# Optimization experiments

Measured on AMD Instinct MI355X. Metric: run time of the kernel, lower is better.

Reference implementation:

```python
import jax, jax.numpy as jnp
import numpy as np

B, S, D = 8, 4096, 1024
H, DH = 16, 64
DM = H * DH  # d_model = 1024


def setup_inputs() -> dict:
    key = jax.random.key(0)
    k0, k1, k2, k3 = jax.random.split(key, 4)
    x = jax.random.uniform(k0, (B, S, D), dtype=jnp.float32)
    # nn.Linear weights (stored here pre-transposed as [in, out]).
    Wq = jax.random.normal(k1, (D, DM), dtype=jnp.float32) * 0.02
    Wkv = jax.random.normal(k2, (D, 2 * DM), dtype=jnp.float32) * 0.02
    Wlin = jax.random.normal(k3, (DM, DM), dtype=jnp.float32) * 0.02
    blin = jnp.zeros((DM,), dtype=jnp.float32)
    return {"x": x, "Wq": Wq, "Wkv": Wkv, "Wlin": Wlin, "blin": blin}


def reference(x, Wq, Wkv, Wlin, blin):
    scale = DH ** (-0.5)
    # projections; cond_dim=None => cond = x (self attention), mask=None
    q = (x @ Wq).reshape(B, S, H, DH)          # [B,S,H,DH]
    kv = (x @ Wkv).reshape(B, S, H, 2 * DH)    # [B,S,H,2*DH]
    k, v = kv[..., :DH], kv[..., DH:]
    # dual softmax: q over feature dim (scaled), k over sequence dim
    q = jax.nn.softmax(q, axis=-1) * scale
    k = jax.nn.softmax(k, axis=1)              # seq axis in BSHD layout
    # context = k^T @ v per (batch, head): [B,H,DH,DH]
    context = jnp.einsum('bshd,bshe->bhde', k, v)
    # out = q @ context: [B,S,H,DH]
    out = jnp.einsum('bshd,bhde->bshe', q, context).reshape(B, S, DM)
    return out @ Wlin + blin
```

## Files before the change

kernel.cpp:

```cpp
#include <hip/hip_runtime.h>
#include <hip/hip_bf16.h>
#include <cstdint>

using bf16 = __hip_bfloat16;
typedef __attribute__((ext_vector_type(8))) short bf16x8;
typedef __attribute__((ext_vector_type(4))) float f32x4;

struct alignas(16) B8 { bf16 h[8]; };
struct alignas(8)  B4 { bf16 h[4]; };

__device__ __forceinline__ void gll16(const void* g, void* l) {
  __builtin_amdgcn_global_load_lds((__attribute__((address_space(1))) void*)g,
                                   (__attribute__((address_space(3))) void*)l,
                                   16, 0, 0);
}

__global__ void cast_f32_bf16(const float* __restrict__ in, bf16* __restrict__ out, long long n) {
  long long i = ((long long)blockIdx.x * blockDim.x + threadIdx.x) * 8;
  if (i >= n) return;
  float4 v0 = *(const float4*)(in + i);
  float4 v1 = *(const float4*)(in + i + 4);
  B8 o;
  o.h[0] = __float2bfloat16(v0.x); o.h[1] = __float2bfloat16(v0.y);
  o.h[2] = __float2bfloat16(v0.z); o.h[3] = __float2bfloat16(v0.w);
  o.h[4] = __float2bfloat16(v1.x); o.h[5] = __float2bfloat16(v1.y);
  o.h[6] = __float2bfloat16(v1.z); o.h[7] = __float2bfloat16(v1.w);
  *(B8*)(out + i) = o;
}

__global__ void tcast(const float* __restrict__ W, bf16* __restrict__ WT, int K, int N) {
  __shared__ float tile[32][33];
  int k0 = blockIdx.y * 32, n0 = blockIdx.x * 32;
  int tx = threadIdx.x, ty = threadIdx.y;
  for (int yy = ty; yy < 32; yy += 8)
    tile[yy][tx] = W[(size_t)(k0 + yy) * N + n0 + tx];
  __syncthreads();
  for (int yy = ty; yy < 32; yy += 8)
    WT[(size_t)(n0 + yy) * K + k0 + tx] = __float2bfloat16(tile[tx][yy]);
}

constexpr int QKV_NT = 12;

__global__ __launch_bounds__(512, 2)
void gemm_qkv(const bf16* __restrict__ A, const bf16* __restrict__ BT,
              bf16* __restrict__ Yq, float* __restrict__ ctxAcc)
{
  __shared__ __align__(16) union {
    struct { bf16 a[4 * 8192]; bf16 b[4 * 8192]; } g;
    struct { bf16 ekT[2][16384]; bf16 vT[2][16384]; } c;
  } sm;

  const int t = threadIdx.x;
  const int wave = t >> 6, lane = t & 63;
  const int lr = lane & 15, kq = lane >> 4;
  const int wm = wave >> 2, wn = wave & 3;
  const int bm = (int)blockIdx.x / QKV_NT, bn = (int)blockIdx.x % QKV_NT;
  const int m0 = bm * 256, n0 = bn * 256;

  const int srow = t >> 2;
  const int cl = (t & 3) ^ ((srow ^ (srow >> 2)) & 3);
  const bf16* aop0 = A + (size_t)(m0 + srow) * 1024 + cl * 8;
  const bf16* aop1 = A + (size_t)(m0 + 128 + srow) * 1024 + cl * 8;
  const bf16* bop0 = BT + (size_t)(n0 + srow) * 1024 + cl * 8;
  const bf16* bop1 = BT + (size_t)(n0 + 128 + srow) * 1024 + cl * 8;
  bf16* const ldsA = sm.g.a;
  bf16* const ldsB = sm.g.b;
  const int wd0 = wave * 512;
  const int wd1 = 4096 + wave * 512;

  const int fc = (kq ^ ((lr ^ (lr >> 2)) & 3)) * 8;
  const int arow = wm * 128 + lr;
  const int brow = wn * 64 + lr;

#define STAGE_A(slot, ko) do { gll16(aop0 + (ko), ldsA + (slot) * 8192 + wd0); \
                               gll16(aop1 + (ko), ldsA + (slot) * 8192 + wd1); } while (0)
#define STAGE_B(slot, ko) do { gll16(bop0 + (ko), ldsB + (slot) * 8192 + wd0); \
                               gll16(bop1 + (ko), ldsB + (slot) * 8192 + wd1); } while (0)
#define AFRAG(slot, i) (*(const bf16x8*)(ldsA + (slot) * 8192 + (arow + (i) * 16) * 32 + fc))
#define BFRAG(slot, j) (*(const bf16x8*)(ldsB + (slot) * 8192 + (brow + (j) * 16) * 32 + fc))

  const f32x4 zero = {0.f, 0.f, 0.f, 0.f};
  f32x4 acc[8][4];
  #pragma unroll
  for (int i = 0; i < 8; i++)
    #pragma unroll
    for (int j = 0; j < 4; j++) acc[i][j] = zero;

  STAGE_A(0, 0); STAGE_B(0, 0);
  STAGE_A(1, 32); STAGE_B(1, 32);
  asm volatile("s_waitcnt vmcnt(4)" ::: "memory");
  __builtin_amdgcn_s_barrier();
  __builtin_amdgcn_sched_barrier(0);

  #pragma unroll 2
  for (int kt = 0; kt < 16; ++kt) {
    const int s0 = (2 * kt) & 3, s1 = (2 * kt + 1) & 3;
    const int p0 = (2 * kt + 2) & 3, p1 = (2 * kt + 3) & 3;
    const int ko = (kt + 1) * 64;
    const bool more = kt < 15;
    bf16x8 a[4], b[4];

    #pragma unroll
    for (int j = 0; j < 4; j++) b[j] = BFRAG(s0, j);
    #pragma unroll
    for (int i = 0; i < 4; i++) a[i] = AFRAG(s0, i);
    if (more) STAGE_A(p0, ko);
    __builtin_amdgcn_s_barrier();
    asm volatile("s_waitcnt lgkmcnt(0)" ::: "memory");
    __builtin_amdgcn_sched_barrier(0);
    __builtin_amdgcn_s_setprio(1);
    #pragma unroll
    for (int i = 0; i < 4; i++)
      #pragma unroll
      for (int j = 0; j < 4; j++)
        acc[i][j] = __builtin_amdgcn_mfma_f32_16x16x32_bf16(a[i], b[j], acc[i][j], 0, 0, 0);
    __builtin_amdgcn_s_setprio(0);
    __builtin_amdgcn_s_barrier();

    #pragma unroll
    for (int i = 0; i < 4; i++) a[i] = AFRAG(s0, i + 4);
    if (more) STAGE_B(p0, ko);
    __builtin_amdgcn_s_barrier();
    asm volatile("s_waitcnt lgkmcnt(0)" ::: "memory");
    __builtin_amdgcn_sched_barrier(0);
    __builtin_amdgcn_s_setprio(1);
    #pragma unroll
    for (int i = 0; i < 4; i++)
      #pragma unroll
      for (int j = 0; j < 4; j++)
        acc[i + 4][j] = __builtin_amdgcn_mfma_f32_16x16x32_bf16(a[i], b[j], acc[i + 4][j], 0, 0, 0);
    __builtin_amdgcn_s_setprio(0);
    if (more) { asm volatile("s_waitcnt vmcnt(4)" ::: "memory"); }
    else      { asm volatile("s_waitcnt vmcnt(0)" ::: "memory"); }
    __builtin_amdgcn_s_barrier();
    __builtin_amdgcn_sched_barrier(0);

    #pragma unroll
    for (int j = 0; j < 4; j++) b[j] = BFRAG(s1, j);
    #pragma unroll
    for (int i = 0; i < 4; i++) a[i] = AFRAG(s1, i);
    if (more) STAGE_A(p1, ko + 32);
    __builtin_amdgcn_s_barrier();
    asm volatile("s_waitcnt lgkmcnt(0)" ::: "memory");
    __builtin_amdgcn_sched_barrier(0);
    __builtin_amdgcn_s_setprio(1);
    #pragma unroll
    for (int i = 0; i < 4; i++)
      #pragma unroll
      for (int j = 0; j < 4; j++)
        acc[i][j] = __builtin_amdgcn_mfma_f32_16x16x32_bf16(a[i], b[j], acc[i][j], 0, 0, 0);
    __builtin_amdgcn_s_setprio(0);
    __builtin_amdgcn_s_barrier();

    #pragma unroll
    for (int i = 0; i < 4; i++) a[i] = AFRAG(s1, i + 4);
    if (more) STAGE_B(p1, ko + 32);
    __builtin_amdgcn_s_barrier();
    asm volatile("s_waitcnt lgkmcnt(0)" ::: "memory");
    __builtin_amdgcn_sched_barrier(0);
    __builtin_amdgcn_s_setprio(1);
    #pragma unroll
    for (int i = 0; i < 4; i++)
      #pragma unroll
      for (int j = 0; j < 4; j++)
        acc[i + 4][j] = __builtin_amdgcn_mfma_f32_16x16x32_bf16(a[i], b[j], acc[i + 4][j], 0, 0, 0);
    __builtin_amdgcn_s_setprio(0);
    if (more) { asm volatile("s_waitcnt vmcnt(4)" ::: "memory"); }
    else      { asm volatile("s_waitcnt vmcnt(0)" ::: "memory"); }
    __builtin_amdgcn_s_barrier();
    __builtin_amdgcn_sched_barrier(0);
  }

  if (bn < 4) {
    #pragma unroll
    for (int i = 0; i < 8; i++) {
      #pragma unroll
      for (int r = 0; r < 4; r++) {
        float m = fmaxf(fmaxf(acc[i][0][r], acc[i][1][r]),
                        fmaxf(acc[i][2][r], acc[i][3][r]));
        m = fmaxf(m, __shfl_xor(m, 1));
        m = fmaxf(m, __shfl_xor(m, 2));
        m = fmaxf(m, __shfl_xor(m, 4));
        m = fmaxf(m, __shfl_xor(m, 8));
        float ex[4]; float s = 0.f;
        #pragma unroll
        for (int j = 0; j < 4; j++) { ex[j] = __expf(acc[i][j][r] - m); s += ex[j]; }
        s += __shfl_xor(s, 1);
        s += __shfl_xor(s, 2);
        s += __shfl_xor(s, 4);
        s += __shfl_xor(s, 8);
        const float inv = 0.125f / s;
        const int row = m0 + wm * 128 + i * 16 + kq * 4 + r;
        bf16* yrow = Yq + (size_t)row * 1024 + n0 + wn * 64;
        #pragma unroll
        for (int j = 0; j < 4; j++)
          yrow[j * 16 + lr] = __float2bfloat16(ex[j] * inv);
      }
    }
  } else {
    const int bb = m0 >> 12;
    const int h0 = (n0 - 1024) >> 7;
    const int hloc = wn >> 1, isV = wn & 1;
    bf16* const dstT = (isV ? sm.c.vT[hloc] : sm.c.ekT[hloc]);

    float zp[4] = {0.f, 0.f, 0.f, 0.f};
    #pragma unroll
    for (int i = 0; i < 8; i++) {
      const int sbase = wm * 128 + i * 16 + kq * 4;
      const int sxo = sbase >> 3;
      const int sby = (sbase & 7) * 2;
      #pragma unroll
      for (int j = 0; j < 4; j++) {
        const int d = j * 16 + lr;
        B4 pk;
        if (!isV) {
          #pragma unroll
          for (int r = 0; r < 4; r++) {
            float e = __expf(acc[i][j][r]);
            zp[j] += e;
            pk.h[r] = __float2bfloat16(e);
          }
        } else {
          #pragma unroll
          for (int r = 0; r < 4; r++) pk.h[r] = __float2bfloat16(acc[i][j][r]);
        }
        *(B4*)((char*)dstT + d * 512 + ((sxo ^ (d & 7)) << 4) + sby) = pk;
      }
    }

    if (!isV) {
      #pragma unroll
      for (int j = 0; j < 4; j++) {
        zp[j] += __shfl_xor(zp[j], 16);
        zp[j] += __shfl_xor(zp[j], 32);
      }
      if (kq == 0) {
        float* zb = ctxAcc + (size_t)(bb * 16 + h0 + hloc) * 4160 + 4096;
        #pragma unroll
        for (int j = 0; j < 4; j++) atomicAdd(zb + j * 16 + lr, zp[j]);
      }
    }
    __syncthreads();

    const int hh = wave >> 2, dq = wave & 3;
    const bf16* const ek = sm.c.ekT[hh];
    const bf16* const vv = sm.c.vT[hh];
    f32x4 racc[4] = {zero, zero, zero, zero};
    #pragma unroll
    for (int ks = 0; ks < 8; ks++) {
      const int ch = ks * 4 + kq;
      bf16x8 af = *(const bf16x8*)((const char*)ek + (dq * 16 + lr) * 512 + ((ch ^ (lr & 7)) << 4));
      #pragma unroll
      for (int j = 0; j < 4; j++) {
        bf16x8 bfr = *(const bf16x8*)((const char*)vv + (j * 16 + lr) * 512 + ((ch ^ (lr & 7)) << 4));
        racc[j] = __builtin_amdgcn_mfma_f32_16x16x32_bf16(af, bfr, racc[j], 0, 0, 0);
      }
    }
    float* cb = ctxAcc + (size_t)(bb * 16 + h0 + hh) * 4160;
    #pragma unroll
    for (int j = 0; j < 4; j++) {
      #pragma unroll
      for (int r = 0; r < 4; r++)
        atomicAdd(cb + (dq * 16 + kq * 4 + r) * 64 + j * 16 + lr, racc[j][r]);
    }
  }
#undef STAGE_A
#undef STAGE_B
#undef AFRAG
#undef BFRAG
}

__global__ __launch_bounds__(256) void ctx_finish(const float* __restrict__ ctxAcc,
                                                  bf16* __restrict__ ctxN) {
  const int bh = blockIdx.x;
  const int t = threadIdx.x;
  __shared__ float zs[64];
  const float* src = ctxAcc + (size_t)bh * 4160;
  if (t < 64) zs[t] = src[4096 + t];
  __syncthreads();
  for (int idx = t; idx < 4096; idx += 256)
    ctxN[(size_t)bh * 4096 + idx] = __float2bfloat16(src[idx] / zs[idx >> 6]);
}

__global__ __launch_bounds__(256) void make_w2t(const bf16* __restrict__ ctxN,
                                                const bf16* __restrict__ WlinT,
                                                bf16* __restrict__ W2T) {
  const int nc = blockIdx.x;
  const int bh = blockIdx.y;
  const int b = bh >> 4, h = bh & 15;
  const int t = threadIdx.x, lane = t & 63, w = t >> 6;
  float creg[64];
  const bf16* crow = ctxN + (size_t)bh * 4096 + lane * 64;
  #pragma unroll
  for (int e8 = 0; e8 < 8; e8++) {
    B8 v = *(const B8*)(crow + e8 * 8);
    #pragma unroll
    for (int j = 0; j < 8; j++) creg[e8 * 8 + j] = __bfloat162float(v.h[j]);
  }
  for (int i = 0; i < 16; i++) {
    const int n = nc * 64 + w * 16 + i;
    const bf16* wrow = WlinT + (size_t)n * 1024 + h * 64;
    float acc = 0.f;
    #pragma unroll
    for (int e8 = 0; e8 < 8; e8++) {
      B8 v = *(const B8*)(wrow + e8 * 8);
      #pragma unroll
      for (int j = 0; j < 8; j++) acc += creg[e8 * 8 + j] * __bfloat162float(v.h[j]);
    }
    W2T[((size_t)b * 1024 + n) * 1024 + h * 64 + lane] = __float2bfloat16(acc);
  }
}

__global__ __launch_bounds__(256)
void gemm_out(const bf16* __restrict__ Aall, const bf16* __restrict__ BTall,
              float* __restrict__ Call, const float* __restrict__ bias)
{
  __shared__ __align__(16) bf16 As[128 * 32];
  __shared__ __align__(16) bf16 Bs[128 * 32];
  const int bz = blockIdx.y;
  const bf16* A  = Aall  + (size_t)bz * 4096 * 1024;
  const bf16* BT = BTall + (size_t)bz * 1024 * 1024;
  float* C       = Call  + (size_t)bz * 4096 * 1024;
  const int nt = 8;
  const int bm = (int)blockIdx.x / nt, bn = (int)blockIdx.x % nt;
  const int m0 = bm * 128, n0 = bn * 128;
  const int t = threadIdx.x;
  const int wave = t >> 6, lane = t & 63;
  const int lr = lane & 15, kq = lane >> 4, kb = kq * 8;
  const int wm = (wave >> 1) * 64, wn = (wave & 1) * 64;

  const int srow = t >> 2;
  const int scol = (t & 3) * 8;
  const bf16* a_src0 = A + (size_t)(m0 + srow) * 1024 + scol;
  const bf16* a_src1 = A + (size_t)(m0 + 64 + srow) * 1024 + scol;
  const bf16* b_src0 = BT + (size_t)(n0 + srow) * 1024 + scol;
  const bf16* b_src1 = BT + (size_t)(n0 + 64 + srow) * 1024 + scol;
  bf16* a_dst0 = As + wave * 512;
  bf16* a_dst1 = As + 2048 + wave * 512;
  bf16* b_dst0 = Bs + wave * 512;
  bf16* b_dst1 = Bs + 2048 + wave * 512;

  f32x4 zero = {0.f, 0.f, 0.f, 0.f};
  f32x4 acc[4][4];
  #pragma unroll
  for (int i = 0; i < 4; i++)
    #pragma unroll
    for (int j = 0; j < 4; j++) acc[i][j] = zero;

  for (int kt = 0; kt < 32; ++kt) {
    __syncthreads();
    gll16(a_src0, a_dst0); gll16(a_src1, a_dst1);
    gll16(b_src0, b_dst0); gll16(b_src1, b_dst1);
    a_src0 += 32; a_src1 += 32; b_src0 += 32; b_src1 += 32;
    __syncthreads();
    bf16x8 a[4], b[4];
    #pragma unroll
    for (int i = 0; i < 4; i++) a[i] = *(const bf16x8*)(As + (wm + i * 16 + lr) * 32 + kb);
    #pragma unroll
    for (int j = 0; j < 4; j++) b[j] = *(const bf16x8*)(Bs + (wn + j * 16 + lr) * 32 + kb);
    #pragma unroll
    for (int i = 0; i < 4; i++)
      #pragma unroll
      for (int j = 0; j < 4; j++)
        acc[i][j] = __builtin_amdgcn_mfma_f32_16x16x32_bf16(a[i], b[j], acc[i][j], 0, 0, 0);
  }

  #pragma unroll
  for (int i = 0; i < 4; i++) {
    const int row0 = m0 + wm + i * 16 + kq * 4;
    #pragma unroll
    for (int j = 0; j < 4; j++) {
      const int col = n0 + wn + j * 16 + lr;
      const float bv = bias[col];
      #pragma unroll
      for (int r = 0; r < 4; r++)
        C[(size_t)(row0 + r) * 1024 + col] = acc[i][j][r] + bv;
    }
  }
}

extern "C" void kernel_launch(void* const* d_in, const int* in_sizes, int n_in,
                              void* d_out, int out_size, void* d_ws, size_t ws_size,
                              hipStream_t stream) {
  (void)in_sizes; (void)n_in; (void)out_size; (void)ws_size;
  const float* x    = (const float*)d_in[0];
  const float* Wq   = (const float*)d_in[1];
  const float* Wkv  = (const float*)d_in[2];
  const float* Wlin = (const float*)d_in[3];
  const float* blin = (const float*)d_in[4];
  float* out = (float*)d_out;

  bf16* x_bf  = (bf16*)d_ws;
  bf16* WTc   = x_bf + 33554432;
  bf16* WlinT = WTc + 3145728;
  bf16* Yq    = WlinT + 1048576;
  bf16* ctxN  = Yq + 33554432;
  bf16* W2T   = ctxN + 524288;
  float* ctxAcc = (float*)(W2T + 8388608);

  cast_f32_bf16<<<16384, 256, 0, stream>>>(x, x_bf, 33554432LL);
  tcast<<<dim3(32, 32), dim3(32, 8), 0, stream>>>(Wq, WTc, 1024, 1024);
  tcast<<<dim3(64, 32), dim3(32, 8), 0, stream>>>(Wkv, WTc + 1048576, 1024, 2048);
  tcast<<<dim3(32, 32), dim3(32, 8), 0, stream>>>(Wlin, WlinT, 1024, 1024);

  hipMemsetAsync(ctxAcc, 0, (size_t)128 * 4160 * sizeof(float), stream);

  gemm_qkv<<<dim3(128 * QKV_NT), 512, 0, stream>>>(x_bf, WTc, Yq, ctxAcc);
  ctx_finish<<<128, 256, 0, stream>>>(ctxAcc, ctxN);
  make_w2t<<<dim3(16, 128), 256, 0, stream>>>(ctxN, WlinT, W2T);
  gemm_out<<<dim3(256, 8), 256, 0, stream>>>(Yq, W2T, out, blin);
}
```

Measured before the change: 439.4 us.

## Reuse pipelined 256x256 GEMM mainloop for output GEMM and fuse ctx normalization

Moves the four-slot, LDS-swizzled 256x256 MFMA mainloop of the QKV GEMM into a shared device function. The output GEMM now uses it with 512 threads, replacing the simple 128x128 tile that synchronised on every k-step. It also drops the ctx_finish kernel: make_w2t reads the fp32 context accumulators and divides by the normaliser inline, which saves a launch and an intermediate buffer. The larger tile launches fewer blocks (512) and uses more LDS and registers per block, so occupancy and wave balance change.

```diff
diff --git a/kernel.cpp b/kernel.cpp
--- a/kernel.cpp
+++ b/kernel.cpp
@@ -39,6 +39,109 @@
     WT[(size_t)(n0 + yy) * K + k0 + tx] = __float2bfloat16(tile[tx][yy]);
 }
 
+__device__ __forceinline__ void gemm_mainloop_256(
+    const bf16* __restrict__ aop0, const bf16* __restrict__ aop1,
+    const bf16* __restrict__ bop0, const bf16* __restrict__ bop1,
+    bf16* ldsA, bf16* ldsB, int wd0, int wd1,
+    int arow, int brow, int fc, f32x4 (&acc)[8][4])
+{
+#define STAGE_A(slot, ko) do { gll16(aop0 + (ko), ldsA + (slot) * 8192 + wd0); \
+                               gll16(aop1 + (ko), ldsA + (slot) * 8192 + wd1); } while (0)
+#define STAGE_B(slot, ko) do { gll16(bop0 + (ko), ldsB + (slot) * 8192 + wd0); \
+                               gll16(bop1 + (ko), ldsB + (slot) * 8192 + wd1); } while (0)
+#define AFRAG(slot, i) (*(const bf16x8*)(ldsA + (slot) * 8192 + (arow + (i) * 16) * 32 + fc))
+#define BFRAG(slot, j) (*(const bf16x8*)(ldsB + (slot) * 8192 + (brow + (j) * 16) * 32 + fc))
+
+  STAGE_A(0, 0); STAGE_B(0, 0);
+  STAGE_A(1, 32); STAGE_B(1, 32);
+  asm volatile("s_waitcnt vmcnt(4)" ::: "memory");
+  __builtin_amdgcn_s_barrier();
+  __builtin_amdgcn_sched_barrier(0);
+
+  #pragma unroll 2
+  for (int kt = 0; kt < 16; ++kt) {
+    const int s0 = (2 * kt) & 3, s1 = (2 * kt + 1) & 3;
+    const int p0 = (2 * kt + 2) & 3, p1 = (2 * kt + 3) & 3;
+    const int ko = (kt + 1) * 64;
+    const bool more = kt < 15;
+    bf16x8 a[4], b[4];
+
+    #pragma unroll
+    for (int j = 0; j < 4; j++) b[j] = BFRAG(s0, j);
+    #pragma unroll
+    for (int i = 0; i < 4; i++) a[i] = AFRAG(s0, i);
+    if (more) STAGE_A(p0, ko);
+    __builtin_amdgcn_s_barrier();
+    asm volatile("s_waitcnt lgkmcnt(0)" ::: "memory");
+    __builtin_amdgcn_sched_barrier(0);
+    __builtin_amdgcn_s_setprio(1);
+    #pragma unroll
+    for (int i = 0; i < 4; i++)
+      #pragma unroll
+      for (int j = 0; j < 4; j++)
+        acc[i][j] = __builtin_amdgcn_mfma_f32_16x16x32_bf16(a[i], b[j], acc[i][j], 0, 0, 0);
+    __builtin_amdgcn_s_setprio(0);
+    __builtin_amdgcn_s_barrier();
+
+    #pragma unroll
+    for (int i = 0; i < 4; i++) a[i] = AFRAG(s0, i + 4);
+    if (more) STAGE_B(p0, ko);
+    __builtin_amdgcn_s_barrier();
+    asm volatile("s_waitcnt lgkmcnt(0)" ::: "memory");
+    __builtin_amdgcn_sched_barrier(0);
+    __builtin_amdgcn_s_setprio(1);
+    #pragma unroll
+    for (int i = 0; i < 4; i++)
+      #pragma unroll
+      for (int j = 0; j < 4; j++)
+        acc[i + 4][j] = __builtin_amdgcn_mfma_f32_16x16x32_bf16(a[i], b[j], acc[i + 4][j], 0, 0, 0);
+    __builtin_amdgcn_s_setprio(0);
+    if (more) { asm volatile("s_waitcnt vmcnt(4)" ::: "memory"); }
+    else      { asm volatile("s_waitcnt vmcnt(0)" ::: "memory"); }
+    __builtin_amdgcn_s_barrier();
+    __builtin_amdgcn_sched_barrier(0);
+
+    #pragma unroll
+    for (int j = 0; j < 4; j++) b[j] = BFRAG(s1, j);
+    #pragma unroll
+    for (int i = 0; i < 4; i++) a[i] = AFRAG(s1, i);
+    if (more) STAGE_A(p1, ko + 32);
+    __builtin_amdgcn_s_barrier();
+    asm volatile("s_waitcnt lgkmcnt(0)" ::: "memory");
+    __builtin_amdgcn_sched_barrier(0);
+    __builtin_amdgcn_s_setprio(1);
+    #pragma unroll
+    for (int i = 0; i < 4; i++)
+      #pragma unroll
+      for (int j = 0; j < 4; j++)
+        acc[i][j] = __builtin_amdgcn_mfma_f32_16x16x32_bf16(a[i], b[j], acc[i][j], 0, 0, 0);
+    __builtin_amdgcn_s_setprio(0);
+    __builtin_amdgcn_s_barrier();
+
+    #pragma unroll
+    for (int i = 0; i < 4; i++) a[i] = AFRAG(s1, i + 4);
+    if (more) STAGE_B(p1, ko + 32);
+    __builtin_amdgcn_s_barrier();
+    asm volatile("s_waitcnt lgkmcnt(0)" ::: "memory");
+    __builtin_amdgcn_sched_barrier(0);
+    __builtin_amdgcn_s_setprio(1);
+    #pragma unroll
+    for (int i = 0; i < 4; i++)
+      #pragma unroll
+      for (int j = 0; j < 4; j++)
+        acc[i + 4][j] = __builtin_amdgcn_mfma_f32_16x16x32_bf16(a[i], b[j], acc[i + 4][j], 0, 0, 0);
+    __builtin_amdgcn_s_setprio(0);
+    if (more) { asm volatile("s_waitcnt vmcnt(4)" ::: "memory"); }
+    else      { asm volatile("s_waitcnt vmcnt(0)" ::: "memory"); }
+    __builtin_amdgcn_s_barrier();
+    __builtin_amdgcn_sched_barrier(0);
+  }
+#undef STAGE_A
+#undef STAGE_B
+#undef AFRAG
+#undef BFRAG
+}
+
 constexpr int QKV_NT = 12;
 
 __global__ __launch_bounds__(512, 2)
@@ -63,8 +166,6 @@
   const bf16* aop1 = A + (size_t)(m0 + 128 + srow) * 1024 + cl * 8;
   const bf16* bop0 = BT + (size_t)(n0 + srow) * 1024 + cl * 8;
   const bf16* bop1 = BT + (size_t)(n0 + 128 + srow) * 1024 + cl * 8;
-  bf16* const ldsA = sm.g.a;
-  bf16* const ldsB = sm.g.b;
   const int wd0 = wave * 512;
   const int wd1 = 4096 + wave * 512;
 
@@ -72,13 +173,6 @@
   const int arow = wm * 128 + lr;
   const int brow = wn * 64 + lr;
 
-#define STAGE_A(slot, ko) do { gll16(aop0 + (ko), ldsA + (slot) * 8192 + wd0); \
-                               gll16(aop1 + (ko), ldsA + (slot) * 8192 + wd1); } while (0)
-#define STAGE_B(slot, ko) do { gll16(bop0 + (ko), ldsB + (slot) * 8192 + wd0); \
-                               gll16(bop1 + (ko), ldsB + (slot) * 8192 + wd1); } while (0)
-#define AFRAG(slot, i) (*(const bf16x8*)(ldsA + (slot) * 8192 + (arow + (i) * 16) * 32 + fc))
-#define BFRAG(slot, j) (*(const bf16x8*)(ldsB + (slot) * 8192 + (brow + (j) * 16) * 32 + fc))
-
   const f32x4 zero = {0.f, 0.f, 0.f, 0.f};
   f32x4 acc[8][4];
   #pragma unroll
@@ -86,90 +180,8 @@
     #pragma unroll
     for (int j = 0; j < 4; j++) acc[i][j] = zero;
 
-  STAGE_A(0, 0); STAGE_B(0, 0);
-  STAGE_A(1, 32); STAGE_B(1, 32);
-  asm volatile("s_waitcnt vmcnt(4)" ::: "memory");
-  __builtin_amdgcn_s_barrier();
-  __builtin_amdgcn_sched_barrier(0);
-
-  #pragma unroll 2
-  for (int kt = 0; kt < 16; ++kt) {
-    const int s0 = (2 * kt) & 3, s1 = (2 * kt + 1) & 3;
-    const int p0 = (2 * kt + 2) & 3, p1 = (2 * kt + 3) & 3;
-    const int ko = (kt + 1) * 64;
-    const bool more = kt < 15;
-    bf16x8 a[4], b[4];
-
-    #pragma unroll
-    for (int j = 0; j < 4; j++) b[j] = BFRAG(s0, j);
-    #pragma unroll
-    for (int i = 0; i < 4; i++) a[i] = AFRAG(s0, i);
-    if (more) STAGE_A(p0, ko);
-    __builtin_amdgcn_s_barrier();
-    asm volatile("s_waitcnt lgkmcnt(0)" ::: "memory");
-    __builtin_amdgcn_sched_barrier(0);
-    __builtin_amdgcn_s_setprio(1);
-    #pragma unroll
-    for (int i = 0; i < 4; i++)
-      #pragma unroll
-      for (int j = 0; j < 4; j++)
-        acc[i][j] = __builtin_amdgcn_mfma_f32_16x16x32_bf16(a[i], b[j], acc[i][j], 0, 0, 0);
-    __builtin_amdgcn_s_setprio(0);
-    __builtin_amdgcn_s_barrier();
-
-    #pragma unroll
-    for (int i = 0; i < 4; i++) a[i] = AFRAG(s0, i + 4);
-    if (more) STAGE_B(p0, ko);
-    __builtin_amdgcn_s_barrier();
-    asm volatile("s_waitcnt lgkmcnt(0)" ::: "memory");
-    __builtin_amdgcn_sched_barrier(0);
-    __builtin_amdgcn_s_setprio(1);
-    #pragma unroll
-    for (int i = 0; i < 4; i++)
-      #pragma unroll
-      for (int j = 0; j < 4; j++)
-        acc[i + 4][j] = __builtin_amdgcn_mfma_f32_16x16x32_bf16(a[i], b[j], acc[i + 4][j], 0, 0, 0);
-    __builtin_amdgcn_s_setprio(0);
-    if (more) { asm volatile("s_waitcnt vmcnt(4)" ::: "memory"); }
-    else      { asm volatile("s_waitcnt vmcnt(0)" ::: "memory"); }
-    __builtin_amdgcn_s_barrier();
-    __builtin_amdgcn_sched_barrier(0);
-
-    #pragma unroll
-    for (int j = 0; j < 4; j++) b[j] = BFRAG(s1, j);
-    #pragma unroll
-    for (int i = 0; i < 4; i++) a[i] = AFRAG(s1, i);
-    if (more) STAGE_A(p1, ko + 32);
-    __builtin_amdgcn_s_barrier();
-    asm volatile("s_waitcnt lgkmcnt(0)" ::: "memory");
-    __builtin_amdgcn_sched_barrier(0);
-    __builtin_amdgcn_s_setprio(1);
-    #pragma unroll
-    for (int i = 0; i < 4; i++)
-      #pragma unroll
-      for (int j = 0; j < 4; j++)
-        acc[i][j] = __builtin_amdgcn_mfma_f32_16x16x32_bf16(a[i], b[j], acc[i][j], 0, 0, 0);
-    __builtin_amdgcn_s_setprio(0);
-    __builtin_amdgcn_s_barrier();
-
-    #pragma unroll
-    for (int i = 0; i < 4; i++) a[i] = AFRAG(s1, i + 4);
-    if (more) STAGE_B(p1, ko + 32);
-    __builtin_amdgcn_s_barrier();
-    asm volatile("s_waitcnt lgkmcnt(0)" ::: "memory");
-    __builtin_amdgcn_sched_barrier(0);
-    __builtin_amdgcn_s_setprio(1);
-    #pragma unroll
-    for (int i = 0; i < 4; i++)
-      #pragma unroll
-      for (int j = 0; j < 4; j++)
-        acc[i + 4][j] = __builtin_amdgcn_mfma_f32_16x16x32_bf16(a[i], b[j], acc[i + 4][j], 0, 0, 0);
-    __builtin_amdgcn_s_setprio(0);
-    if (more) { asm volatile("s_waitcnt vmcnt(4)" ::: "memory"); }
-    else      { asm volatile("s_waitcnt vmcnt(0)" ::: "memory"); }
-    __builtin_amdgcn_s_barrier();
-    __builtin_amdgcn_sched_barrier(0);
-  }
+  gemm_mainloop_256(aop0, aop1, bop0, bop1, sm.g.a, sm.g.b, wd0, wd1,
+                    arow, brow, fc, acc);
 
   if (bn < 4) {
     #pragma unroll
@@ -264,38 +276,24 @@
         atomicAdd(cb + (dq * 16 + kq * 4 + r) * 64 + j * 16 + lr, racc[j][r]);
     }
   }
-#undef STAGE_A
-#undef STAGE_B
-#undef AFRAG
-#undef BFRAG
-}
-
-__global__ __launch_bounds__(256) void ctx_finish(const float* __restrict__ ctxAcc,
-                                                  bf16* __restrict__ ctxN) {
-  const int bh = blockIdx.x;
-  const int t = threadIdx.x;
-  __shared__ float zs[64];
-  const float* src = ctxAcc + (size_t)bh * 4160;
-  if (t < 64) zs[t] = src[4096 + t];
-  __syncthreads();
-  for (int idx = t; idx < 4096; idx += 256)
-    ctxN[(size_t)bh * 4096 + idx] = __float2bfloat16(src[idx] / zs[idx >> 6]);
-}
-
-__global__ __launch_bounds__(256) void make_w2t(const bf16* __restrict__ ctxN,
+}
+
+__global__ __launch_bounds__(256) void make_w2t(const float* __restrict__ ctxAcc,
                                                 const bf16* __restrict__ WlinT,
                                                 bf16* __restrict__ W2T) {
   const int nc = blockIdx.x;
   const int bh = blockIdx.y;
   const int b = bh >> 4, h = bh & 15;
   const int t = threadIdx.x, lane = t & 63, w = t >> 6;
+  const float* src = ctxAcc + (size_t)bh * 4160;
+  const float invz = 1.0f / src[4096 + lane];
   float creg[64];
-  const bf16* crow = ctxN + (size_t)bh * 4096 + lane * 64;
-  #pragma unroll
-  for (int e8 = 0; e8 < 8; e8++) {
-    B8 v = *(const B8*)(crow + e8 * 8);
-    #pragma unroll
-    for (int j = 0; j < 8; j++) creg[e8 * 8 + j] = __bfloat162float(v.h[j]);
+  const float* crow = src + lane * 64;
+  #pragma unroll
+  for (int e4 = 0; e4 < 16; e4++) {
+    float4 v = *(const float4*)(crow + e4 * 4);
+    creg[e4 * 4 + 0] = v.x * invz; creg[e4 * 4 + 1] = v.y * invz;
+    creg[e4 * 4 + 2] = v.z * invz; creg[e4 * 4 + 3] = v.w * invz;
   }
   for (int i = 0; i < 16; i++) {
     const int n = nc * 64 + w * 16 + i;
@@ -311,70 +309,57 @@
   }
 }
 
-__global__ __launch_bounds__(256)
+__global__ __launch_bounds__(512, 2)
 void gemm_out(const bf16* __restrict__ Aall, const bf16* __restrict__ BTall,
               float* __restrict__ Call, const float* __restrict__ bias)
 {
-  __shared__ __align__(16) bf16 As[128 * 32];
-  __shared__ __align__(16) bf16 Bs[128 * 32];
+  __shared__ __align__(16) struct { bf16 a[4 * 8192]; bf16 b[4 * 8192]; } sm;
+  const int t = threadIdx.x;
+  const int wave = t >> 6, lane = t & 63;
+  const int lr = lane & 15, kq = lane >> 4;
+  const int wm = wave >> 2, wn = wave & 3;
   const int bz = blockIdx.y;
+  const int bm = (int)blockIdx.x >> 2, bn = (int)blockIdx.x & 3;
+  const int m0 = bm * 256, n0 = bn * 256;
   const bf16* A  = Aall  + (size_t)bz * 4096 * 1024;
   const bf16* BT = BTall + (size_t)bz * 1024 * 1024;
   float* C       = Call  + (size_t)bz * 4096 * 1024;
-  const int nt = 8;
-  const int bm = (int)blockIdx.x / nt, bn = (int)blockIdx.x % nt;
-  const int m0 = bm * 128, n0 = bn * 128;
-  const int t = threadIdx.x;
-  const int wave = t >> 6, lane = t & 63;
-  const int lr = lane & 15, kq = lane >> 4, kb = kq * 8;
-  const int wm = (wave >> 1) * 64, wn = (wave & 1) * 64;
 
   const int srow = t >> 2;
-  const int scol = (t & 3) * 8;
-  const bf16* a_src0 = A + (size_t)(m0 + srow) * 1024 + scol;
-  const bf16* a_src1 = A + (size_t)(m0 + 64 + srow) * 1024 + scol;
-  const bf16* b_src0 = BT + (size_t)(n0 + srow) * 1024 + scol;
-  const bf16* b_src1 = BT + (size_t)(n0 + 64 + srow) * 1024 + scol;
-  bf16* a_dst0 = As + wave * 512;
-  bf16* a_dst1 = As + 2048 + wave * 512;
-  bf16* b_dst0 = Bs + wave * 512;
-  bf16* b_dst1 = Bs + 2048 + wave * 512;
-
-  f32x4 zero = {0.f, 0.f, 0.f, 0.f};
-  f32x4 acc[4][4];
-  #pragma unroll
-  for (int i = 0; i < 4; i++)
+  const int cl = (t & 3) ^ ((srow ^ (srow >> 2)) & 3);
+  const bf16* aop0 = A + (size_t)(m0 + srow) * 1024 + cl * 8;
+  const bf16* aop1 = A + (size_t)(m0 + 128 + srow) * 1024 + cl * 8;
+  const bf16* bop0 = BT + (size_t)(n0 + srow) * 1024 + cl * 8;
+  const bf16* bop1 = BT + (size_t)(n0 + 128 + srow) * 1024 + cl * 8;
+  const int wd0 = wave * 512;
+  const int wd1 = 4096 + wave * 512;
+
+  const int fc = (kq ^ ((lr ^ (lr >> 2)) & 3)) * 8;
+  const int arow = wm * 128 + lr;
+  const int brow = wn * 64 + lr;
+
+  const f32x4 zero = {0.f, 0.f, 0.f, 0.f};
+  f32x4 acc[8][4];
+  #pragma unroll
+  for (int i = 0; i < 8; i++)
     #pragma unroll
     for (int j = 0; j < 4; j++) acc[i][j] = zero;
 
-  for (int kt = 0; kt < 32; ++kt) {
-    __syncthreads();
-    gll16(a_src0, a_dst0); gll16(a_src1, a_dst1);
-    gll16(b_src0, b_dst0); gll16(b_src1, b_dst1);
-    a_src0 += 32; a_src1 += 32; b_src0 += 32; b_src1 += 32;
-    __syncthreads();
-    bf16x8 a[4], b[4];
-    #pragma unroll
-    for (int i = 0; i < 4; i++) a[i] = *(const bf16x8*)(As + (wm + i * 16 + lr) * 32 + kb);
-    #pragma unroll
-    for (int j = 0; j < 4; j++) b[j] = *(const bf16x8*)(Bs + (wn + j * 16 + lr) * 32 + kb);
-    #pragma unroll
-    for (int i = 0; i < 4; i++)
-      #pragma unroll
-      for (int j = 0; j < 4; j++)
-        acc[i][j] = __builtin_amdgcn_mfma_f32_16x16x32_bf16(a[i], b[j], acc[i][j], 0, 0, 0);
-  }
-
-  #pragma unroll
-  for (int i = 0; i < 4; i++) {
-    const int row0 = m0 + wm + i * 16 + kq * 4;
+  gemm_mainloop_256(aop0, aop1, bop0, bop1, sm.a, sm.b, wd0, wd1,
+                    arow, brow, fc, acc);
+
+  float bv[4];
+  #pragma unroll
+  for (int j = 0; j < 4; j++) bv[j] = bias[n0 + wn * 64 + j * 16 + lr];
+  #pragma unroll
+  for (int i = 0; i < 8; i++) {
+    const int row0 = m0 + wm * 128 + i * 16 + kq * 4;
     #pragma unroll
     for (int j = 0; j < 4; j++) {
-      const int col = n0 + wn + j * 16 + lr;
-      const float bv = bias[col];
+      const int col = n0 + wn * 64 + j * 16 + lr;
       #pragma unroll
       for (int r = 0; r < 4; r++)
-        C[(size_t)(row0 + r) * 1024 + col] = acc[i][j][r] + bv;
+        C[(size_t)(row0 + r) * 1024 + col] = acc[i][j][r] + bv[j];
     }
   }
 }
@@ -394,8 +379,7 @@
   bf16* WTc   = x_bf + 33554432;
   bf16* WlinT = WTc + 3145728;
   bf16* Yq    = WlinT + 1048576;
-  bf16* ctxN  = Yq + 33554432;
-  bf16* W2T   = ctxN + 524288;
+  bf16* W2T   = Yq + 33554432;
   float* ctxAcc = (float*)(W2T + 8388608);
 
   cast_f32_bf16<<<16384, 256, 0, stream>>>(x, x_bf, 33554432LL);
@@ -406,7 +390,6 @@
   hipMemsetAsync(ctxAcc, 0, (size_t)128 * 4160 * sizeof(float), stream);
 
   gemm_qkv<<<dim3(128 * QKV_NT), 512, 0, stream>>>(x_bf, WTc, Yq, ctxAcc);
-  ctx_finish<<<128, 256, 0, stream>>>(ctxAcc, ctxN);
-  make_w2t<<<dim3(16, 128), 256, 0, stream>>>(ctxN, WlinT, W2T);
-  gemm_out<<<dim3(256, 8), 256, 0, stream>>>(Yq, W2T, out, blin);
-}
+  make_w2t<<<dim3(16, 128), 256, 0, stream>>>(ctxAcc, WlinT, W2T);
+  gemm_out<<<dim3(64, 8), 512, 0, stream>>>(Yq, W2T, out, blin);
+}
```

After: 418.7 us. 4.7% less time.
